# Optimization experiments

Measured on AMD Instinct MI355X. Metric: run time of the kernel, lower is better.

The kernel has to match this reference:

```python
import jax, jax.numpy as jnp
import numpy as np

DIM = 1024
NUM_HEADS = 16
HEAD_DIM = DIM // NUM_HEADS
SCALE = HEAD_DIM ** -0.5


def setup_inputs() -> dict:
    key = jax.random.key(0)
    k_x, k_wqkv, k_bqkv, k_wp, k_bp = jax.random.split(key, 5)
    B, C, D = 4, 1024, DIM
    x = jax.random.normal(k_x, (B, C, D), dtype=jnp.float32)
    # nn.Linear stores weight as (out, in); we keep (in, out) for x @ W
    w_qkv = jax.random.normal(k_wqkv, (D, 3 * D), dtype=jnp.float32) * (D ** -0.5)
    b_qkv = jax.random.normal(k_bqkv, (3 * D,), dtype=jnp.float32) * 0.02
    w_proj = jax.random.normal(k_wp, (D, D), dtype=jnp.float32) * (D ** -0.5)
    b_proj = jax.random.normal(k_bp, (D,), dtype=jnp.float32) * 0.02
    return {"x": x, "w_qkv": w_qkv, "b_qkv": b_qkv, "w_proj": w_proj, "b_proj": b_proj}


def reference(x, w_qkv, b_qkv, w_proj, b_proj):
    B, C, D = x.shape
    H, Hd = NUM_HEADS, HEAD_DIM
    qkv = x @ w_qkv + b_qkv                       # (B, C, 3D)
    qkv = qkv.reshape(B, C, 3, H, Hd)
    q = qkv[:, :, 0].transpose(0, 2, 1, 3)        # (B, H, C, Hd)
    k = qkv[:, :, 1].transpose(0, 2, 1, 3)
    v = qkv[:, :, 2].transpose(0, 2, 1, 3)
    attn = jnp.einsum('bhqd,bhkd->bhqk', q, k) * SCALE
    attn = jax.nn.softmax(attn, axis=-1)
    out = jnp.einsum('bhqk,bhkd->bhqd', attn, v)  # (B, H, C, Hd)
    out = out.transpose(0, 2, 1, 3).reshape(B, C, D)
    return out @ w_proj + b_proj
```

## Files before the change

### kernel.cpp

```cpp
#include <hip/hip_runtime.h>
#include <cstdint>

#define BB 4
#define CC 1024
#define DD 1024
#define HH 16
#define HD 64
#define NH3 3072

typedef __attribute__((ext_vector_type(8))) short short8;
typedef __attribute__((ext_vector_type(4))) float f32x4;

#define MFMA16(a, b, c) __builtin_amdgcn_mfma_f32_16x16x32_bf16(a, b, c, 0, 0, 0)
#define EXP2 __builtin_amdgcn_exp2f

__device__ __forceinline__ void glds16(const void* g, void* l) {
    __builtin_amdgcn_global_load_lds(
        (const __attribute__((address_space(1))) void*)g,
        (__attribute__((address_space(3))) void*)l, 16, 0, 0);
}

__device__ __forceinline__ ushort f2bf(float f) {
    union { float f; uint32_t u; } v; v.f = f;
    uint32_t r = v.u + 0x7FFF + ((v.u >> 16) & 1);
    return (ushort)(r >> 16);
}

__device__ __forceinline__ uint32_t pack2bf(float a, float b) {
    uint32_t ua = __float_as_uint(a), ub = __float_as_uint(b);
    ua += 0x7FFF + ((ua >> 16) & 1);
    ub += 0x7FFF + ((ub >> 16) & 1);
    return __builtin_amdgcn_perm(ua, ub, 0x03020706);
}

__global__ __launch_bounds__(256)
void prep_kernel(const float* __restrict__ x, ushort* __restrict__ xbf,
                 const float* __restrict__ wqkv, ushort* __restrict__ wqkvT,
                 const float* __restrict__ wprj, ushort* __restrict__ wprjT)
{
    __shared__ float Ts[64 * 65];
    const int blk = blockIdx.x;
    const int t = threadIdx.x;

    if (blk < 4096) {
        int i = blk * 256 + t;
        float4 v = ((const float4*)x)[i];
        ushort4 o;
        o.x = f2bf(v.x); o.y = f2bf(v.y); o.z = f2bf(v.z); o.w = f2bf(v.w);
        ((ushort4*)xbf)[i] = o;
        return;
    }

    const float* in; ushort* outp; int K, N, n0, k0;
    if (blk < 4864) {
        int bx = blk - 4096;
        in = wqkv; outp = wqkvT; K = DD; N = NH3;
        n0 = (bx % 48) * 64; k0 = (bx / 48) * 64;
    } else {
        int bx = blk - 4864;
        in = wprj; outp = wprjT; K = DD; N = DD;
        n0 = (bx % 16) * 64; k0 = (bx / 16) * 64;
    }
    #pragma unroll
    for (int i = 0; i < 16; ++i) {
        int idx = t + i * 256;
        int r = idx >> 6, c = idx & 63;
        Ts[r * 65 + c] = in[(size_t)(k0 + r) * N + n0 + c];
    }
    __syncthreads();
    #pragma unroll
    for (int i = 0; i < 16; ++i) {
        int idx = t + i * 256;
        int rr = idx >> 6, cc = idx & 63;
        outp[(size_t)(n0 + rr) * K + k0 + cc] = f2bf(Ts[cc * 65 + rr]);
    }
}

template<int MODE, int MT>
__global__ __launch_bounds__(256)
void gemm_bt(const ushort* __restrict__ A, const ushort* __restrict__ Bt,
             const float* __restrict__ bias, float* __restrict__ Cf,
             ushort* __restrict__ qb, ushort* __restrict__ kb, ushort* __restrict__ vtb,
             int M, int N, int K)
{
    constexpr int MI = MT / 32;
    __shared__ ushort As[2][MT * 32];
    __shared__ ushort Bs[2][128 * 32];

    const int tid = threadIdx.x;
    const int wid = tid >> 6, lane = tid & 63;
    const int quad = lane >> 4, l15 = lane & 15;
    const int m0 = blockIdx.y * MT, n0 = blockIdx.x * 128;
    const int wm = (wid >> 1) * (MT / 2), wn = (wid & 1) * 64;

    const int sr = lane >> 2;
    const int sc = lane & 3;

    const int ar0 = wid * (MT / 4) + sr;
    const int acg0 = sc ^ ((ar0 >> 1) & 3);
    const int acg1 = sc ^ (((ar0 + 16) >> 1) & 3);
    const ushort* Ar0 = A + (size_t)(m0 + ar0) * K + acg0 * 8;
    const ushort* Ar1 = A + (size_t)(m0 + ar0 + 16) * K + acg1 * 8;
    const int br0 = wid * 32 + sr;
    const int bcg0 = sc ^ ((br0 >> 1) & 3);
    const int bcg1 = sc ^ (((br0 + 16) >> 1) & 3);
    const ushort* Br0 = Bt + (size_t)(n0 + br0) * K + bcg0 * 8;
    const ushort* Br1 = Bt + (size_t)(n0 + br0 + 16) * K + bcg1 * 8;

    f32x4 acc[MI][4];
    #pragma unroll
    for (int i = 0; i < MI; ++i)
        #pragma unroll
        for (int j = 0; j < 4; ++j) acc[i][j] = (f32x4)(0.0f);

    glds16(Ar0, &As[0][(wid * (MT / 4)) * 32]);
    glds16(Br0, &Bs[0][(wid * 32) * 32]);
    if (MT == 128) glds16(Ar1, &As[0][(wid * 32 + 16) * 32]);
    glds16(Br1, &Bs[0][(wid * 32 + 16) * 32]);

    int buf = 0;
    for (int k0 = 0; k0 < K; k0 += 32) {
        __syncthreads();
        if (k0 + 32 < K) {
            const int kn = k0 + 32;
            glds16(Ar0 + kn, &As[buf ^ 1][(wid * (MT / 4)) * 32]);
            glds16(Br0 + kn, &Bs[buf ^ 1][(wid * 32) * 32]);
            if (MT == 128) glds16(Ar1 + kn, &As[buf ^ 1][(wid * 32 + 16) * 32]);
            glds16(Br1 + kn, &Bs[buf ^ 1][(wid * 32 + 16) * 32]);
        }

        short8 af[MI], bf[4];
        #pragma unroll
        for (int i = 0; i < MI; ++i) {
            int row = wm + i * 16 + l15;
            af[i] = *(const short8*)(&As[buf][row * 32 + (quad ^ ((row >> 1) & 3)) * 8]);
        }
        #pragma unroll
        for (int j = 0; j < 4; ++j) {
            int col = wn + j * 16 + l15;
            bf[j] = *(const short8*)(&Bs[buf][col * 32 + (quad ^ ((col >> 1) & 3)) * 8]);
        }
        #pragma unroll
        for (int i = 0; i < MI; ++i)
            #pragma unroll
            for (int j = 0; j < 4; ++j)
                acc[i][j] = MFMA16(af[i], bf[j], acc[i][j]);
        buf ^= 1;
    }

    if (MODE == 0) {
        #pragma unroll
        for (int i = 0; i < MI; ++i) {
            int row = m0 + wm + i * 16 + quad * 4;
            #pragma unroll
            for (int j = 0; j < 4; ++j) {
                int col = n0 + wn + j * 16 + l15;
                float bv = bias[col];
                #pragma unroll
                for (int r = 0; r < 4; ++r)
                    Cf[(size_t)(row + r) * N + col] = acc[i][j][r] + bv;
            }
        }
    } else {
        #pragma unroll
        for (int j = 0; j < 4; ++j) {
            int n = n0 + wn + j * 16 + l15;
            int three = n >> 10;
            int h = (n >> 6) & 15;
            int hd = n & 63;
            float scale = (three == 0) ? 0.1803368801f : 1.0f;
            float bv = bias[n];
            #pragma unroll
            for (int i = 0; i < MI; ++i) {
                int row = m0 + wm + i * 16 + quad * 4;
                #pragma unroll
                for (int r = 0; r < 4; ++r) {
                    int m = row + r;
                    int b = m >> 10, c = m & 1023;
                    ushort val = f2bf((acc[i][j][r] + bv) * scale);
                    if (three == 0)
                        qb[((size_t)((b * HH + h) * CC) + c) * HD + hd] = val;
                    else if (three == 1)
                        kb[((size_t)((b * HH + h) * CC) + c) * HD + hd] = val;
                    else
                        vtb[((size_t)((b * HH + h) * HD) + hd) * CC + c] = val;
                }
            }
        }
    }
}

__global__ __launch_bounds__(512, 2)
void gemm_qkv256(const ushort* __restrict__ A, const ushort* __restrict__ Bt,
                 const float* __restrict__ bias,
                 ushort* __restrict__ qb, ushort* __restrict__ kb,
                 ushort* __restrict__ vtb)
{
    constexpr int K  = DD;
    constexpr int KT = K / 32;
    __shared__ ushort lds[4][16384];

    const int tid = threadIdx.x;
    const int wid = tid >> 6, lane = tid & 63;
    const int quad = lane >> 4, l15 = lane & 15;
    const int m0 = blockIdx.y * 256, n0 = blockIdx.x * 256;
    const int wm = (wid >> 2) * 128, wn = (wid & 3) * 64;

    const int sr = lane >> 2, sc = lane & 3;
    const int ra = wid * 16 + sr;
    const int cga = sc ^ ((ra >> 1) & 3);
    const ushort* Ap0 = A  + (size_t)(m0 + ra) * K + cga * 8;
    const ushort* Ap1 = Ap0 + (size_t)128 * K;
    const ushort* Bp0 = Bt + (size_t)(n0 + ra) * K + cga * 8;
    const ushort* Bp1 = Bp0 + (size_t)128 * K;
    const int sA0 = (wid * 16) * 32;
    const int sA1 = sA0 + 128 * 32;
    const int sB0 = 8192 + sA0;
    const int sB1 = 8192 + sA1;

#define QSTAGE(kt) do { ushort* lb_ = &lds[(kt) & 3][0]; const int ko_ = (kt) * 32; \
        glds16(Ap0 + ko_, lb_ + sA0); \
        glds16(Ap1 + ko_, lb_ + sA1); \
        glds16(Bp0 + ko_, lb_ + sB0); \
        glds16(Bp1 + ko_, lb_ + sB1); } while (0)

    f32x4 acc[8][4];
    #pragma unroll
    for (int i = 0; i < 8; ++i)
        #pragma unroll
        for (int j = 0; j < 4; ++j) acc[i][j] = (f32x4)(0.0f);

    QSTAGE(0); QSTAGE(1); QSTAGE(2);

#define QPHASE(kt, VMS, DOSTAGE) do { \
        asm volatile("s_waitcnt " VMS "\n\ts_barrier" ::: "memory"); \
        const ushort* ab_ = &lds[(kt) & 3][0]; \
        short8 af_[8], bf_[4]; \
        _Pragma("unroll") \
        for (int i = 0; i < 8; ++i) { \
            int row = wm + i * 16 + l15; \
            af_[i] = *(const short8*)(ab_ + row * 32 + (quad ^ ((row >> 1) & 3)) * 8); } \
        _Pragma("unroll") \
        for (int j = 0; j < 4; ++j) { \
            int col = wn + j * 16 + l15; \
            bf_[j] = *(const short8*)(ab_ + 8192 + col * 32 + (quad ^ ((col >> 1) & 3)) * 8); } \
        if (DOSTAGE) QSTAGE((kt) + 3); \
        __builtin_amdgcn_s_setprio(1); \
        _Pragma("unroll") \
        for (int i = 0; i < 8; ++i) \
            _Pragma("unroll") \
            for (int j = 0; j < 4; ++j) \
                acc[i][j] = MFMA16(af_[i], bf_[j], acc[i][j]); \
        __builtin_amdgcn_s_setprio(0); \
        __builtin_amdgcn_sched_barrier(0); \
    } while (0)

    #pragma unroll 4
    for (int kt = 0; kt < KT - 4; ++kt)
        QPHASE(kt, "vmcnt(8)", true);
    QPHASE(KT - 4, "vmcnt(8)", true);
    QPHASE(KT - 3, "vmcnt(8)", false);
    QPHASE(KT - 2, "vmcnt(4)", false);
    QPHASE(KT - 1, "vmcnt(0)", false);

    #pragma unroll
    for (int j = 0; j < 4; ++j) {
        int n = n0 + wn + j * 16 + l15;
        int three = n >> 10;
        int h = (n >> 6) & 15;
        int hd = n & 63;
        float scale = (three == 0) ? 0.1803368801f : 1.0f;
        float bv = bias[n];
        #pragma unroll
        for (int i = 0; i < 8; ++i) {
            int row = m0 + wm + i * 16 + quad * 4;
            #pragma unroll
            for (int r = 0; r < 4; ++r) {
                int m = row + r;
                int b = m >> 10, c = m & 1023;
                ushort val = f2bf((acc[i][j][r] + bv) * scale);
                if (three == 0)
                    qb[((size_t)((b * HH + h) * CC) + c) * HD + hd] = val;
                else if (three == 1)
                    kb[((size_t)((b * HH + h) * CC) + c) * HD + hd] = val;
                else
                    vtb[((size_t)((b * HH + h) * HD) + hd) * CC + c] = val;
            }
        }
    }
#undef QPHASE
#undef QSTAGE
}

__global__ __launch_bounds__(256)
void attn_mfma6(const ushort* __restrict__ qb, const ushort* __restrict__ kb,
                const ushort* __restrict__ vt, ushort* __restrict__ attnb)
{
    __shared__ ushort lds[2 * 4096 + 3 * 4096 + 2 * 9216];
    const uint K0 = 0, K1 = 4096;
    const uint V0 = 8192, V1 = 12288, V2 = 16384;
    const uint P0 = 20480, P1 = 29696;

    const int tid = threadIdx.x;
    const int wid = tid >> 6, lane = tid & 63;
    const int quad = lane >> 4, l15 = lane & 15;
    const int bh = blockIdx.x & 63;
    const int qt = blockIdx.x >> 6;
    const int q0 = qt * 128;
    const int b = bh >> 4, h = bh & 15;

    const ushort* Qp  = qb + ((size_t)bh * CC + q0) * HD;
    const ushort* Kp  = kb + (size_t)bh * CC * HD;
    const ushort* Vtp = vt + (size_t)bh * HD * CC;

    const int sr = lane >> 3;
    const int sc = lane & 7;

    short8 qf[2][2];
    #pragma unroll
    for (int q2 = 0; q2 < 2; ++q2) {
        int row = wid * 32 + q2 * 16 + l15;
        #pragma unroll
        for (int s = 0; s < 2; ++s)
            qf[q2][s] = *(const short8*)(Qp + (size_t)row * HD + (s * 4 + quad) * 8);
    }

    const int kr = wid * 16 + sr;
    const int cgA = sc ^ (kr & 7);
    const int cgB = sc ^ ((kr + 8) & 7);
    const ushort* Kr0 = Kp  + (size_t)kr * HD + cgA * 8;
    const ushort* Kr1 = Kp  + (size_t)(kr + 8) * HD + cgB * 8;
    const ushort* Vr0 = Vtp + (size_t)kr * CC + cgA * 8;
    const ushort* Vr1 = Vtp + (size_t)(kr + 8) * CC + cgB * 8;

    const uint stg0 = (wid * 16) * 64;
    const uint stg1 = (wid * 16 + 8) * 64;

    glds16(Kr0, lds + K0 + stg0);
    glds16(Kr1, lds + K0 + stg1);
    glds16(Vr0, lds + V0 + stg0);
    glds16(Vr1, lds + V0 + stg1);

    f32x4 oacc[2][4];
    #pragma unroll
    for (int q2 = 0; q2 < 2; ++q2)
        #pragma unroll
        for (int hb = 0; hb < 4; ++hb) oacc[q2][hb] = (f32x4)(0.0f);
    float lsum[2] = {0.0f, 0.0f};

    uint ksC = K0, ksN = K1;
    uint vsP = V2, vsC = V0, vsN = V1;
    uint psC = P0, psP = P1;

    for (int kt = 0; kt < 16; ++kt) {
        __syncthreads();
        if (kt < 15) {
            const int koff = (kt + 1) * 64;
            glds16(Kr0 + (size_t)koff * HD, lds + ksN + stg0);
            glds16(Kr1 + (size_t)koff * HD, lds + ksN + stg1);
            glds16(Vr0 + koff,              lds + vsN + stg0);
            glds16(Vr1 + koff,              lds + vsN + stg1);
        }

        if (kt > 0) {
            short8 vf[4][2];
            #pragma unroll
            for (int hb = 0; hb < 4; ++hb) {
                int hr = hb * 16 + l15;
                vf[hb][0] = *(const short8*)(lds + vsP + hr * 64 + ((quad ^ (hr & 7)) * 8));
                vf[hb][1] = *(const short8*)(lds + vsP + hr * 64 + (((4 + quad) ^ (hr & 7)) * 8));
            }
            #pragma unroll
            for (int q2 = 0; q2 < 2; ++q2) {
                int row = wid * 32 + q2 * 16 + l15;
                short8 pf0 = *(const short8*)(lds + psP + row * 72 + quad * 8);
                short8 pf1 = *(const short8*)(lds + psP + row * 72 + 32 + quad * 8);
                #pragma unroll
                for (int hb = 0; hb < 4; ++hb) {
                    oacc[q2][hb] = MFMA16(pf0, vf[hb][0], oacc[q2][hb]);
                    oacc[q2][hb] = MFMA16(pf1, vf[hb][1], oacc[q2][hb]);
                }
            }
        }

        #pragma unroll
        for (int kb2 = 0; kb2 < 4; ++kb2) {
            int krow = kb2 * 16 + l15;
            short8 kf0 = *(const short8*)(lds + ksC + krow * 64 + ((quad ^ (krow & 7)) * 8));
            short8 kf1 = *(const short8*)(lds + ksC + krow * 64 + (((4 + quad) ^ (krow & 7)) * 8));
            #pragma unroll
            for (int q2 = 0; q2 < 2; ++q2) {
                f32x4 st = (f32x4)(0.0f);
                st = MFMA16(kf0, qf[q2][0], st);
                st = MFMA16(kf1, qf[q2][1], st);
                float p0 = EXP2(st[0]);
                float p1 = EXP2(st[1]);
                float p2 = EXP2(st[2]);
                float p3 = EXP2(st[3]);
                lsum[q2] += (p0 + p1) + (p2 + p3);
                int row = wid * 32 + q2 * 16 + l15;
                *(uint2*)(lds + psC + row * 72 + kb2 * 16 + quad * 4) =
                    make_uint2(pack2bf(p0, p1), pack2bf(p2, p3));
            }
        }

        uint t = vsP; vsP = vsC; vsC = vsN; vsN = t;
        t = ksC; ksC = ksN; ksN = t;
        t = psP; psP = psC; psC = t;
    }

    {
        short8 vf[4][2];
        #pragma unroll
        for (int hb = 0; hb < 4; ++hb) {
            int hr = hb * 16 + l15;
            vf[hb][0] = *(const short8*)(lds + vsP + hr * 64 + ((quad ^ (hr & 7)) * 8));
            vf[hb][1] = *(const short8*)(lds + vsP + hr * 64 + (((4 + quad) ^ (hr & 7)) * 8));
        }
        #pragma unroll
        for (int q2 = 0; q2 < 2; ++q2) {
            int row = wid * 32 + q2 * 16 + l15;
            short8 pf0 = *(const short8*)(lds + psP + row * 72 + quad * 8);
            short8 pf1 = *(const short8*)(lds + psP + row * 72 + 32 + quad * 8);
            #pragma unroll
            for (int hb = 0; hb < 4; ++hb) {
                oacc[q2][hb] = MFMA16(pf0, vf[hb][0], oacc[q2][hb]);
                oacc[q2][hb] = MFMA16(pf1, vf[hb][1], oacc[q2][hb]);
            }
        }
    }

    #pragma unroll
    for (int q2 = 0; q2 < 2; ++q2) {
        lsum[q2] += __shfl_xor(lsum[q2], 16);
        lsum[q2] += __shfl_xor(lsum[q2], 32);
    }

    #pragma unroll
    for (int q2 = 0; q2 < 2; ++q2) {
        #pragma unroll
        for (int r = 0; r < 4; ++r) {
            float inv = 1.0f / __shfl(lsum[q2], (lane & 48) | (quad * 4 + r));
            int c = q0 + wid * 32 + q2 * 16 + quad * 4 + r;
            #pragma unroll
            for (int hb = 0; hb < 4; ++hb) {
                int d = h * 64 + hb * 16 + l15;
                attnb[((size_t)(b * CC + c)) * DD + d] = f2bf(oacc[q2][hb][r] * inv);
            }
        }
    }
}

extern "C" void kernel_launch(void* const* d_in, const int* in_sizes, int n_in,
                              void* d_out, int out_size, void* d_ws, size_t ws_size,
                              hipStream_t stream)
{
    (void)in_sizes; (void)n_in; (void)out_size; (void)ws_size;
    const float* x      = (const float*)d_in[0];
    const float* w_qkv  = (const float*)d_in[1];
    const float* b_qkv  = (const float*)d_in[2];
    const float* w_proj = (const float*)d_in[3];
    const float* b_proj = (const float*)d_in[4];
    float* out = (float*)d_out;

    ushort* p = (ushort*)d_ws;
    ushort* xbf   = p;  p += (size_t)4 * 1024 * 1024;
    ushort* wqkvT = p;  p += (size_t)3 * 1024 * 1024;
    ushort* wprjT = p;  p += (size_t)1 * 1024 * 1024;
    ushort* qbuf  = p;  p += (size_t)4 * 1024 * 1024;
    ushort* kbuf  = p;  p += (size_t)4 * 1024 * 1024;
    ushort* vtb   = p;  p += (size_t)4 * 1024 * 1024;
    ushort* attnb = p;  p += (size_t)4 * 1024 * 1024;

    prep_kernel<<<5120, 256, 0, stream>>>(x, xbf, w_qkv, wqkvT, w_proj, wprjT);

    gemm_qkv256<<<dim3(NH3 / 256, (BB * CC) / 256), 512, 0, stream>>>(
        xbf, wqkvT, b_qkv, qbuf, kbuf, vtb);

    attn_mfma6<<<512, 256, 0, stream>>>(qbuf, kbuf, vtb, attnb);

    gemm_bt<0, 64><<<dim3(DD / 128, (BB * CC) / 64), 256, 0, stream>>>(
        attnb, wprjT, b_proj, out, nullptr, nullptr, nullptr, BB * CC, DD, DD);
}
```

Measured before the change: 192.6 us.

## Split QKV GEMM k-step into four sub-phases interleaving LDS reads, loads, and MFMAs

```diff
diff --git a/kernel.cpp b/kernel.cpp
--- a/kernel.cpp
+++ b/kernel.cpp
@@ -232,36 +232,75 @@
 
     QSTAGE(0); QSTAGE(1); QSTAGE(2);
 
-#define QPHASE(kt, VMS, DOSTAGE) do { \
+#define SCHED0 __builtin_amdgcn_sched_barrier(0)
+
+#define QITER(kt, VMS, DOSTAGE) do { \
         asm volatile("s_waitcnt " VMS "\n\ts_barrier" ::: "memory"); \
         const ushort* ab_ = &lds[(kt) & 3][0]; \
-        short8 af_[8], bf_[4]; \
-        _Pragma("unroll") \
-        for (int i = 0; i < 8; ++i) { \
-            int row = wm + i * 16 + l15; \
-            af_[i] = *(const short8*)(ab_ + row * 32 + (quad ^ ((row >> 1) & 3)) * 8); } \
-        _Pragma("unroll") \
-        for (int j = 0; j < 4; ++j) { \
-            int col = wn + j * 16 + l15; \
-            bf_[j] = *(const short8*)(ab_ + 8192 + col * 32 + (quad ^ ((col >> 1) & 3)) * 8); } \
-        if (DOSTAGE) QSTAGE((kt) + 3); \
+        ushort* nb_ = &lds[((kt) + 3) & 3][0]; \
+        const int ko_ = ((kt) + 3) * 32; \
+        short8 a0_[4], a1_[4], b0_[2], b1_[2]; \
+         \
+        _Pragma("unroll") \
+        for (int i = 0; i < 4; ++i) { int row = wm + i * 16 + l15; \
+            a0_[i] = *(const short8*)(ab_ + row * 32 + (quad ^ ((row >> 1) & 3)) * 8); } \
+        _Pragma("unroll") \
+        for (int j = 0; j < 2; ++j) { int col = wn + j * 16 + l15; \
+            b0_[j] = *(const short8*)(ab_ + 8192 + col * 32 + (quad ^ ((col >> 1) & 3)) * 8); } \
+        if (DOSTAGE) glds16(Ap0 + ko_, nb_ + sA0); \
+        SCHED0; __builtin_amdgcn_s_barrier(); \
         __builtin_amdgcn_s_setprio(1); \
         _Pragma("unroll") \
-        for (int i = 0; i < 8; ++i) \
+        for (int i = 0; i < 4; ++i) \
             _Pragma("unroll") \
-            for (int j = 0; j < 4; ++j) \
-                acc[i][j] = MFMA16(af_[i], bf_[j], acc[i][j]); \
-        __builtin_amdgcn_s_setprio(0); \
-        __builtin_amdgcn_sched_barrier(0); \
+            for (int j = 0; j < 2; ++j) \
+                acc[i][j] = MFMA16(a0_[i], b0_[j], acc[i][j]); \
+        __builtin_amdgcn_s_setprio(0); SCHED0; \
+         \
+        _Pragma("unroll") \
+        for (int j = 0; j < 2; ++j) { int col = wn + (2 + j) * 16 + l15; \
+            b1_[j] = *(const short8*)(ab_ + 8192 + col * 32 + (quad ^ ((col >> 1) & 3)) * 8); } \
+        if (DOSTAGE) glds16(Ap1 + ko_, nb_ + sA1); \
+        SCHED0; __builtin_amdgcn_s_barrier(); \
+        __builtin_amdgcn_s_setprio(1); \
+        _Pragma("unroll") \
+        for (int i = 0; i < 4; ++i) \
+            _Pragma("unroll") \
+            for (int j = 0; j < 2; ++j) \
+                acc[i][2 + j] = MFMA16(a0_[i], b1_[j], acc[i][2 + j]); \
+        __builtin_amdgcn_s_setprio(0); SCHED0; \
+         \
+        _Pragma("unroll") \
+        for (int i = 0; i < 4; ++i) { int row = wm + (4 + i) * 16 + l15; \
+            a1_[i] = *(const short8*)(ab_ + row * 32 + (quad ^ ((row >> 1) & 3)) * 8); } \
+        if (DOSTAGE) glds16(Bp0 + ko_, nb_ + sB0); \
+        SCHED0; __builtin_amdgcn_s_barrier(); \
+        __builtin_amdgcn_s_setprio(1); \
+        _Pragma("unroll") \
+        for (int i = 0; i < 4; ++i) \
+            _Pragma("unroll") \
+            for (int j = 0; j < 2; ++j) \
+                acc[4 + i][j] = MFMA16(a1_[i], b0_[j], acc[4 + i][j]); \
+        __builtin_amdgcn_s_setprio(0); SCHED0; \
+         \
+        if (DOSTAGE) glds16(Bp1 + ko_, nb_ + sB1); \
+        SCHED0; __builtin_amdgcn_s_barrier(); \
+        __builtin_amdgcn_s_setprio(1); \
+        _Pragma("unroll") \
+        for (int i = 0; i < 4; ++i) \
+            _Pragma("unroll") \
+            for (int j = 0; j < 2; ++j) \
+                acc[4 + i][2 + j] = MFMA16(a1_[i], b1_[j], acc[4 + i][2 + j]); \
+        __builtin_amdgcn_s_setprio(0); SCHED0; \
     } while (0)
 
     #pragma unroll 4
     for (int kt = 0; kt < KT - 4; ++kt)
-        QPHASE(kt, "vmcnt(8)", true);
-    QPHASE(KT - 4, "vmcnt(8)", true);
-    QPHASE(KT - 3, "vmcnt(8)", false);
-    QPHASE(KT - 2, "vmcnt(4)", false);
-    QPHASE(KT - 1, "vmcnt(0)", false);
+        QITER(kt, "vmcnt(8)", true);
+    QITER(KT - 4, "vmcnt(8)", true);
+    QITER(KT - 3, "vmcnt(8)", false);
+    QITER(KT - 2, "vmcnt(4)", false);
+    QITER(KT - 1, "vmcnt(0)", false);
 
     #pragma unroll
     for (int j = 0; j < 4; ++j) {
@@ -288,8 +327,9 @@
             }
         }
     }
-#undef QPHASE
+#undef QITER
 #undef QSTAGE
+#undef SCHED0
 }
 
 __global__ __launch_bounds__(256)
```

Measured after the change: 191.0 us. No clear change (-0.9%).
